# Kernel tuning notes

Measured on AMD Instinct MI355X. Metric: run time of the kernel, lower is better.

Reference implementation:

```python
import jax, jax.numpy as jnp
import numpy as np

N_DIST, H, W, K = 256, 256, 192, 129
DR, DR0, DELTA = 0.2, 0.2, 1e-11


def _dual_exp(d, b1, b2, b3, b4):
    return b1 * np.exp(-b2 * d) + b3 * np.exp(-b4 * d)


def setup_inputs() -> dict:
    key = jax.random.key(0)
    d = (np.arange(N_DIST) + 1.0) * DR                      # distances (cm)
    gaus_amp = _dual_exp(d, 1.0, 0.01, 0.1, 0.001)
    gaus_sig = 0.05 * d + 1.0
    bkg_amp = _dual_exp(d, 0.05, 0.05, 0.01, 0.005)
    bkg_sig = 0.08 * d + 2.0
    xk = np.arange(-(K // 2), K // 2 + 1) * DR / DR0        # (K,) kernel coords
    # gaussian kernel (get_gaus_layer)
    kernel_g = np.sqrt(gaus_amp)[:, None] * np.exp(-xk[None, :] ** 2 / (2 * gaus_sig[:, None] ** 2 + DELTA))
    # background kernels (get_bkg_layers) with emulated splines
    w_f = lambda t: np.exp(-np.abs(t))
    iso_f = lambda t: 1.0 / (1.0 + t ** 2)
    xw = xk[None, :] / bkg_sig[:, None]
    kernel_w = bkg_amp[:, None] * (DR / DR0) * w_f(xw)
    kernel_iso = bkg_amp[:, None] * (DR / DR0) * iso_f(xw)
    # normalization factor (configure)
    xs = np.linspace(-5.0, 5.0, 2001)
    Iw = np.trapz(w_f(xs), xs)
    Iiso = np.trapz(iso_f(xs), xs)
    Nw = 3 * bkg_amp * Iw * bkg_sig
    Niso = bkg_amp * Iiso * bkg_sig
    Ng2 = gaus_amp * 2 * np.pi * gaus_sig ** 2 * (DR0 / DR) ** 2
    norm = (Nw + Niso ** 2 + 1.0) * Ng2
    x = jax.random.uniform(key, (1, N_DIST, H, W), dtype=jnp.float32)
    return {
        "x": x,
        "kernel_g": jnp.asarray(kernel_g, jnp.float32),
        "kernel_w": jnp.asarray(kernel_w, jnp.float32),
        "kernel_iso": jnp.asarray(kernel_iso, jnp.float32),
        "norm": jnp.asarray(norm, jnp.float32),
    }


def _dwconv(x, kern, axis):
    """Depthwise 'same' Conv1d along `axis` of (N,H,W); channels = dim 0."""
    n = x.shape[0]
    perm = (2, 0, 1) if axis == 1 else (1, 0, 2)   # -> (batch, channels=N, length)
    inv = (1, 2, 0) if axis == 1 else (1, 0, 2)
    xb = jnp.transpose(x, perm)
    y = jax.lax.conv_general_dilated(
        xb, kern[:, None, :], (1,), 'SAME',
        feature_group_count=n, dimension_numbers=('NCH', 'OIH', 'NCH'))
    return jnp.transpose(y, inv)


def _rotate(x, ang):
    """Bilinear rotation of (N,S,S) in dims (1,2), zero padding (grid_sample-like)."""
    s = x.shape[1]
    c = (s - 1) * 0.5
    ca, sa = jnp.cos(ang), jnp.sin(ang)
    idx = jnp.arange(s, dtype=x.dtype) - c
    yy, xx = jnp.meshgrid(idx, idx, indexing='ij')
    sy = ca * yy + sa * xx + c   # inverse-rotated source coords
    sx = -sa * yy + ca * xx + c
    y0 = jnp.floor(sy)
    x0 = jnp.floor(sx)
    fy, fx = sy - y0, sx - x0
    y0i, x0i = y0.astype(jnp.int32), x0.astype(jnp.int32)

    def gat(yi, xi):
        valid = (yi >= 0) & (yi < s) & (xi >= 0) & (xi < s)
        v = x[:, jnp.clip(yi, 0, s - 1), jnp.clip(xi, 0, s - 1)]
        return jnp.where(valid, v, 0.0)

    return (gat(y0i, x0i) * (1 - fy) * (1 - fx)
            + gat(y0i, x0i + 1) * (1 - fy) * fx
            + gat(y0i + 1, x0i) * fy * (1 - fx)
            + gat(y0i + 1, x0i + 1) * fy * fx)


def reference(x, kernel_g, kernel_w, kernel_iso, norm):
    out = x[0]                                   # (N, H, W)
    out = _dwconv(out, kernel_g, 1)
    out = _dwconv(out, kernel_g, 2)
    iso = _dwconv(out, kernel_iso, 1)
    iso = _dwconv(iso, kernel_iso, 2)
    n, h, w = out.shape
    pad = (n - w) // 2
    padded = jnp.pad(out, ((0, 0), (0, 0), (pad, pad)))  # (N, H, H) square plane
    tails = jnp.zeros_like(padded)
    for i in range(3):                            # 0, 60, 120 degrees
        ang = float(np.deg2rad(60 * i))
        t = _rotate(padded, ang)
        t = _dwconv(t, kernel_w, 2)
        tails = tails + _rotate(t, -ang)
    tails = tails[:, :, pad:pad + w]
    out = (out + tails + iso) / norm[:, None, None]
    return out[None]
```

## Files before the change

kernel.cpp:

```cpp
#include <hip/hip_runtime.h>
#include <cmath>

#define CN   256
#define HN   256
#define WN   192
#define KN   129
#define RN   64
#define SN   256
#define PADN 32

template <int WD, bool ACC>
__global__ __launch_bounds__(256, 5) void conv_w_lds(const float* __restrict__ in,
                                                     const float* __restrict__ kern,
                                                     float* __restrict__ out) {
    constexpr int PITCH = 97;
    __shared__ float lds[64 * PITCH + 132];
    float* __restrict__ ldsK = lds + 64 * PITCH;
    const int tid = threadIdx.x;
    const int x0  = blockIdx.x * 64;
    const int h0  = blockIdx.y * 64;
    const int c   = blockIdx.z;
    const float* __restrict__ in_c = in + ((size_t)c * HN + h0) * WD;

    if (tid < 132) ldsK[tid] = (tid < KN) ? kern[c * KN + tid] : 0.f;

    const int wv = tid >> 6;
    const int l  = tid & 63;
    const int base  = l * PITCH + wv * 16;
    const int col32 = tid & 31;
    const int r8    = tid >> 5;

    float acc[16];
#pragma unroll
    for (int t = 0; t < 16; ++t) acc[t] = 0.f;

#pragma unroll 1
    for (int s = 0; s < 4; ++s) {
        __syncthreads();
        const int off = x0 + 32 * s - 64;
        if (off >= 0 && off + 96 <= WD) {
#pragma unroll
            for (int m = 0; m < 3; ++m)
#pragma unroll
                for (int k = 0; k < 8; ++k)
                    lds[(r8 + 8 * k) * PITCH + col32 + 32 * m] =
                        in_c[(size_t)(r8 + 8 * k) * WD + off + col32 + 32 * m];
        } else {
#pragma unroll
            for (int m = 0; m < 3; ++m)
#pragma unroll
                for (int k = 0; k < 8; ++k) {
                    int g  = off + col32 + 32 * m;
                    int gc = min(max(g, 0), WD - 1);
                    float v = in_c[(size_t)(r8 + 8 * k) * WD + gc];
                    lds[(r8 + 8 * k) * PITCH + col32 + 32 * m] = (g == gc) ? v : 0.f;
                }
        }
        __syncthreads();

        float H0[16], H1[16], H2[16];
#pragma unroll
        for (int i = 0; i < 16; ++i) H0[i] = lds[base + i];
#pragma unroll
        for (int i = 0; i < 16; ++i) H1[i] = lds[base + 16 + i];

        const float4* __restrict__ k4 = (const float4*)ldsK;
        float4 kc = k4[8 * s];
#pragma unroll
        for (int q = 0; q < 8; ++q) {
            float4 kn = (q < 7) ? k4[8 * s + q + 1] : kc;
#pragma unroll
            for (int u = 0; u < 4; ++u) {
                const int up = 4 * q + u;
                const float kj = (u == 0) ? kc.x : (u == 1) ? kc.y
                               : (u == 2) ? kc.z : kc.w;
#pragma unroll
                for (int t = 0; t < 16; ++t) {
                    const int e = up + t;
                    const float val = (e < 16) ? H0[e]
                                    : (e < 32) ? H1[e - 16] : H2[e - 32];
                    acc[t] = fmaf(val, kj, acc[t]);
                }
            }
            if (q == 0) {
#pragma unroll
                for (int i = 0; i < 16; ++i) H2[i] = lds[base + 32 + i];
            }
            kc = kn;
        }
        if (s == 3) {
            const float k128 = ldsK[128];
#pragma unroll
            for (int t = 0; t < 16; ++t) acc[t] = fmaf(H2[t], k128, acc[t]);
        }
    }

    float4* __restrict__ o4 =
        (float4*)(out + ((size_t)c * HN + h0 + l) * WD + x0 + wv * 16);
#pragma unroll
    for (int q = 0; q < 4; ++q) {
        float4 v;
        v.x = acc[4*q]; v.y = acc[4*q+1]; v.z = acc[4*q+2]; v.w = acc[4*q+3];
        if (ACC) {
            float4 o = o4[q];
            v.x += o.x; v.y += o.y; v.z += o.z; v.w += o.w;
        }
        o4[q] = v;
    }
}

__global__ __launch_bounds__(256, 5) void conv_h_lds(const float* __restrict__ in,
                                                     const float* __restrict__ kern,
                                                     float* __restrict__ out) {
    __shared__ float lds[96 * 64 + 132];
    float* __restrict__ ldsK = lds + 96 * 64;
    const int tid = threadIdx.x;
    const int x0  = blockIdx.x * 64;
    const int h0  = blockIdx.y * 64;
    const int c   = blockIdx.z;
    const float* __restrict__ in_c = in + (size_t)c * HN * WN + x0;

    if (tid < 132) ldsK[tid] = (tid < KN) ? kern[c * KN + tid] : 0.f;

    const int wv = tid >> 6;
    const int l  = tid & 63;
    const int baseRow = wv * 16;
    const int col = tid & 63;
    const int r4  = tid >> 6;

    float acc[16];
#pragma unroll
    for (int t = 0; t < 16; ++t) acc[t] = 0.f;

#pragma unroll 1
    for (int s = 0; s < 4; ++s) {
        __syncthreads();
        const int off = h0 + 32 * s - 64;
        if (off >= 0 && off + 96 <= HN) {
#pragma unroll
            for (int k = 0; k < 24; ++k)
                lds[(r4 + 4 * k) * 64 + col] =
                    in_c[(size_t)(off + r4 + 4 * k) * WN + col];
        } else {
#pragma unroll
            for (int k = 0; k < 24; ++k) {
                int g  = off + r4 + 4 * k;
                int gc = min(max(g, 0), HN - 1);
                float v = in_c[(size_t)gc * WN + col];
                lds[(r4 + 4 * k) * 64 + col] = (g == gc) ? v : 0.f;
            }
        }
        __syncthreads();

        float H0[16], H1[16], H2[16];
#pragma unroll
        for (int i = 0; i < 16; ++i) H0[i] = lds[(baseRow + i) * 64 + l];
#pragma unroll
        for (int i = 0; i < 16; ++i) H1[i] = lds[(baseRow + 16 + i) * 64 + l];

        const float4* __restrict__ k4 = (const float4*)ldsK;
        float4 kc = k4[8 * s];
#pragma unroll
        for (int q = 0; q < 8; ++q) {
            float4 kn = (q < 7) ? k4[8 * s + q + 1] : kc;
#pragma unroll
            for (int u = 0; u < 4; ++u) {
                const int up = 4 * q + u;
                const float kj = (u == 0) ? kc.x : (u == 1) ? kc.y
                               : (u == 2) ? kc.z : kc.w;
#pragma unroll
                for (int t = 0; t < 16; ++t) {
                    const int e = up + t;
                    const float val = (e < 16) ? H0[e]
                                    : (e < 32) ? H1[e - 16] : H2[e - 32];
                    acc[t] = fmaf(val, kj, acc[t]);
                }
            }
            if (q == 0) {
#pragma unroll
                for (int i = 0; i < 16; ++i)
                    H2[i] = lds[(baseRow + 32 + i) * 64 + l];
            }
            kc = kn;
        }
        if (s == 3) {
            const float k128 = ldsK[128];
#pragma unroll
            for (int t = 0; t < 16; ++t) acc[t] = fmaf(H2[t], k128, acc[t]);
        }
    }

    float* __restrict__ ob = out + ((size_t)c * HN + h0 + wv * 16) * WN + x0 + l;
#pragma unroll
    for (int t = 0; t < 16; ++t) ob[(size_t)t * WN] = acc[t];
}

__global__ __launch_bounds__(256) void rot_fwd_k(const float* __restrict__ Cin,
                                                 float* __restrict__ out,
                                                 float ca, float sa) {
    const int jb = blockIdx.x * 128 + threadIdx.x;
    const int i  = blockIdx.y * 8 + threadIdx.y;
    const int c  = blockIdx.z;
    const float cc = (SN - 1) * 0.5f;
    const float yy = (float)i - cc;
    const float* __restrict__ base = Cin + (size_t)c * HN * WN;
    float* __restrict__ orow = out + ((size_t)c * SN + i) * SN;
#pragma unroll
    for (int q = 0; q < 4; ++q) {
        const int j = jb + q * 32;
        float xx = (float)j - cc;
        float sy = ca * yy + sa * xx + cc;
        float sx = -sa * yy + ca * xx + cc;
        float y0f = floorf(sy), x0f = floorf(sx);
        float fy = sy - y0f, fx = sx - x0f;
        int y0 = (int)y0f, x0i = (int)x0f;
        int p  = x0i - PADN;
        int y0c = min(max(y0, 0), HN - 1);
        int y1c = min(max(y0 + 1, 0), HN - 1);
        int p0c = min(max(p, 0), WN - 1);
        int p1c = min(max(p + 1, 0), WN - 1);
        float wy0 = ((unsigned)y0       < (unsigned)HN) ? (1.f - fy) : 0.f;
        float wy1 = ((unsigned)(y0 + 1) < (unsigned)HN) ? fy : 0.f;
        float wx0 = ((unsigned)p        < (unsigned)WN) ? (1.f - fx) : 0.f;
        float wx1 = ((unsigned)(p + 1)  < (unsigned)WN) ? fx : 0.f;
        const float* r0 = base + (size_t)y0c * WN;
        const float* r1 = base + (size_t)y1c * WN;
        float v00 = r0[p0c], v01 = r0[p1c];
        float v10 = r1[p0c], v11 = r1[p1c];
        orow[j] = wy0 * (wx0 * v00 + wx1 * v01) + wy1 * (wx0 * v10 + wx1 * v11);
    }
}

__global__ __launch_bounds__(256) void rot_bwd_k(const float* __restrict__ U,
                                                 float* __restrict__ acc,
                                                 float ca, float sa) {
    const int xb = blockIdx.x * 64 + threadIdx.x;
    const int i  = blockIdx.y * 8 + threadIdx.y;
    const int c  = blockIdx.z;
    const float cc = (SN - 1) * 0.5f;
    const float yy = (float)i - cc;
    const float* __restrict__ base = U + (size_t)c * SN * SN;
    float* __restrict__ arow = acc + ((size_t)c * HN + i) * WN;
#pragma unroll
    for (int q = 0; q < 2; ++q) {
        const int xc = xb + q * 32;
        const int j  = xc + PADN;
        float xx = (float)j - cc;
        float sy = ca * yy + sa * xx + cc;
        float sx = -sa * yy + ca * xx + cc;
        float y0f = floorf(sy), x0f = floorf(sx);
        float fy = sy - y0f, fx = sx - x0f;
        int y0 = (int)y0f, x0i = (int)x0f;
        int y0c = min(max(y0, 0), SN - 1);
        int y1c = min(max(y0 + 1, 0), SN - 1);
        int p0c = min(max(x0i, 0), SN - 1);
        int p1c = min(max(x0i + 1, 0), SN - 1);
        float wy0 = ((unsigned)y0        < (unsigned)SN) ? (1.f - fy) : 0.f;
        float wy1 = ((unsigned)(y0 + 1)  < (unsigned)SN) ? fy : 0.f;
        float wx0 = ((unsigned)x0i       < (unsigned)SN) ? (1.f - fx) : 0.f;
        float wx1 = ((unsigned)(x0i + 1) < (unsigned)SN) ? fx : 0.f;
        const float* r0 = base + (size_t)y0c * SN;
        const float* r1 = base + (size_t)y1c * SN;
        float v00 = r0[p0c], v01 = r0[p1c];
        float v10 = r1[p0c], v11 = r1[p1c];
        arow[xc] += wy0 * (wx0 * v00 + wx1 * v01) + wy1 * (wx0 * v10 + wx1 * v11);
    }
}

__global__ __launch_bounds__(256) void final_k(float* __restrict__ outC,
                                               const float* __restrict__ acc,
                                               const float* __restrict__ norm) {
    size_t i4 = (size_t)blockIdx.x * 256 + threadIdx.x;
    int c = (int)(i4 / (HN * WN / 4));
    float4* o4 = (float4*)outC;
    const float4* a4 = (const float4*)acc;
    float inv = 1.f / norm[c];
    float4 o = o4[i4], a = a4[i4];
    o.x = (o.x + a.x) * inv; o.y = (o.y + a.y) * inv;
    o.z = (o.z + a.z) * inv; o.w = (o.w + a.w) * inv;
    o4[i4] = o;
}

extern "C" void kernel_launch(void* const* d_in, const int* in_sizes, int n_in,
                              void* d_out, int out_size, void* d_ws, size_t ws_size,
                              hipStream_t stream) {
    const float* x    = (const float*)d_in[0];
    const float* kg   = (const float*)d_in[1];
    const float* kw   = (const float*)d_in[2];
    const float* kiso = (const float*)d_in[3];
    const float* norm = (const float*)d_in[4];

    float* C = (float*)d_out;
    float* ws = (float*)d_ws;
    const size_t IMG = (size_t)CN * HN * WN;
    const size_t PSQ = (size_t)CN * SN * SN;
    float* B   = ws;
    float* acc = ws + IMG;
    float* T   = ws + 2 * IMG;
    float* U   = T + PSQ;

    const dim3 blk256(256);
    const dim3 convHGrid(WN / 64, HN / 64, CN);
    const dim3 convW192Grid(WN / 64, HN / 64, CN);
    const dim3 convW256Grid(SN / 64, HN / 64, CN);
    const dim3 rotFGrid(SN / 128, SN / 8, CN), rotBlk(32, 8);
    const dim3 rotBGrid(WN / 64, SN / 8, CN);

    conv_h_lds<<<convHGrid, blk256, 0, stream>>>(x, kg, B);
    conv_w_lds<WN, false><<<convW192Grid, blk256, 0, stream>>>(B, kg, C);
    conv_h_lds<<<convHGrid, blk256, 0, stream>>>(C, kiso, B);
    conv_w_lds<WN, false><<<convW192Grid, blk256, 0, stream>>>(B, kiso, acc);
    conv_w_lds<WN, true><<<convW192Grid, blk256, 0, stream>>>(C, kw, acc);
    const double a1 = 60.0 * M_PI / 180.0, a2 = 120.0 * M_PI / 180.0;
    const float c1 = (float)cos(a1), s1 = (float)sin(a1);
    const float c2 = (float)cos(a2), s2 = (float)sin(a2);

    rot_fwd_k<<<rotFGrid, rotBlk, 0, stream>>>(C, T, c1, s1);
    conv_w_lds<SN, false><<<convW256Grid, blk256, 0, stream>>>(T, kw, U);
    rot_bwd_k<<<rotBGrid, rotBlk, 0, stream>>>(U, acc, c1, -s1);

    rot_fwd_k<<<rotFGrid, rotBlk, 0, stream>>>(C, T, c2, s2);
    conv_w_lds<SN, false><<<convW256Grid, blk256, 0, stream>>>(T, kw, U);
    rot_bwd_k<<<rotBGrid, rotBlk, 0, stream>>>(U, acc, c2, -s2);

    final_k<<<(unsigned)(IMG / 4 / 256), blk256, 0, stream>>>(C, acc, norm);
    (void)in_sizes; (void)n_in; (void)out_size; (void)ws_size;
}
```

Measured before the change: 823.6 us.

## Stage rotation source tiles in LDS and fuse final normalization into last rotation

Rotation kernels now process 64x64 output tiles per block and first stage the rotated footprint (a 92x96 bounding box) of the source plane into shared memory. The bilinear taps are then read from LDS instead of as scattered global loads. The separate final normalization pass is folded into the second backward rotation, which saves one full read/write pass over the image. In exchange, each block loads some padding and boundary elements it never uses, and LDS use per block goes up.

```diff
diff --git a/kernel.cpp b/kernel.cpp
--- a/kernel.cpp
+++ b/kernel.cpp
@@ -8,6 +8,9 @@
 #define RN   64
 #define SN   256
 #define PADN 32
+
+#define BBR 92
+#define BBP 96
 
 template <int WD, bool ACC>
 __global__ __launch_bounds__(256, 5) void conv_w_lds(const float* __restrict__ in,
@@ -195,90 +198,118 @@
     for (int t = 0; t < 16; ++t) ob[(size_t)t * WN] = acc[t];
 }
 
-__global__ __launch_bounds__(256) void rot_fwd_k(const float* __restrict__ Cin,
-                                                 float* __restrict__ out,
-                                                 float ca, float sa) {
-    const int jb = blockIdx.x * 128 + threadIdx.x;
-    const int i  = blockIdx.y * 8 + threadIdx.y;
+__global__ __launch_bounds__(256) void rot_fwd_lds(const float* __restrict__ Cin,
+                                                   float* __restrict__ out,
+                                                   float ca, float sa) {
+    __shared__ float tile[BBR * BBP];
+    const int j0 = blockIdx.x * 64;
+    const int i0 = blockIdx.y * 64;
     const int c  = blockIdx.z;
     const float cc = (SN - 1) * 0.5f;
-    const float yy = (float)i - cc;
+    const float yA = (float)i0 - cc, yB = (float)(i0 + 63) - cc;
+    const float xA = (float)j0 - cc, xB = (float)(j0 + 63) - cc;
+    const float syAA = ca * yA + sa * xA + cc, syAB = ca * yA + sa * xB + cc;
+    const float syBA = ca * yB + sa * xA + cc, syBB = ca * yB + sa * xB + cc;
+    const float sxAA = -sa * yA + ca * xA + cc, sxAB = -sa * yA + ca * xB + cc;
+    const float sxBA = -sa * yB + ca * xA + cc, sxBB = -sa * yB + ca * xB + cc;
+    const int ybase = (int)floorf(fminf(fminf(syAA, syAB), fminf(syBA, syBB))) - 1;
+    const int xbase = (int)floorf(fminf(fminf(sxAA, sxAB), fminf(sxBA, sxBB))) - 1;
+
     const float* __restrict__ base = Cin + (size_t)c * HN * WN;
-    float* __restrict__ orow = out + ((size_t)c * SN + i) * SN;
-#pragma unroll
-    for (int q = 0; q < 4; ++q) {
-        const int j = jb + q * 32;
-        float xx = (float)j - cc;
-        float sy = ca * yy + sa * xx + cc;
-        float sx = -sa * yy + ca * xx + cc;
-        float y0f = floorf(sy), x0f = floorf(sx);
-        float fy = sy - y0f, fx = sx - x0f;
-        int y0 = (int)y0f, x0i = (int)x0f;
-        int p  = x0i - PADN;
-        int y0c = min(max(y0, 0), HN - 1);
-        int y1c = min(max(y0 + 1, 0), HN - 1);
-        int p0c = min(max(p, 0), WN - 1);
-        int p1c = min(max(p + 1, 0), WN - 1);
-        float wy0 = ((unsigned)y0       < (unsigned)HN) ? (1.f - fy) : 0.f;
-        float wy1 = ((unsigned)(y0 + 1) < (unsigned)HN) ? fy : 0.f;
-        float wx0 = ((unsigned)p        < (unsigned)WN) ? (1.f - fx) : 0.f;
-        float wx1 = ((unsigned)(p + 1)  < (unsigned)WN) ? fx : 0.f;
-        const float* r0 = base + (size_t)y0c * WN;
-        const float* r1 = base + (size_t)y1c * WN;
-        float v00 = r0[p0c], v01 = r0[p1c];
-        float v10 = r1[p0c], v11 = r1[p1c];
-        orow[j] = wy0 * (wx0 * v00 + wx1 * v01) + wy1 * (wx0 * v10 + wx1 * v11);
-    }
-}
-
-__global__ __launch_bounds__(256) void rot_bwd_k(const float* __restrict__ U,
-                                                 float* __restrict__ acc,
-                                                 float ca, float sa) {
-    const int xb = blockIdx.x * 64 + threadIdx.x;
-    const int i  = blockIdx.y * 8 + threadIdx.y;
+    for (int t = threadIdx.x; t < BBR * BBP; t += 256) {
+        const int r  = t / BBP;
+        const int q  = t - r * BBP;
+        const int gy = ybase + r;
+        const int gx = xbase + q - PADN;
+        float v = 0.f;
+        if ((unsigned)gy < (unsigned)HN && (unsigned)gx < (unsigned)WN)
+            v = base[(size_t)gy * WN + gx];
+        tile[t] = v;
+    }
+    __syncthreads();
+
+    const int l  = threadIdx.x & 63;
+    const int r0 = threadIdx.x >> 6;
+    const int j  = j0 + l;
+    const float xx = (float)j - cc;
+    float* __restrict__ ocol = out + (size_t)c * SN * SN + j;
+#pragma unroll
+    for (int t = 0; t < 16; ++t) {
+        const int i = i0 + r0 + 4 * t;
+        const float yy = (float)i - cc;
+        const float sy = ca * yy + sa * xx + cc;
+        const float sx = -sa * yy + ca * xx + cc;
+        const float y0f = floorf(sy), x0f = floorf(sx);
+        const float fy = sy - y0f, fx = sx - x0f;
+        const int ly = (int)y0f - ybase;
+        const int lx = (int)x0f - xbase;
+        const float* p = tile + ly * BBP + lx;
+        const float v00 = p[0], v01 = p[1], v10 = p[BBP], v11 = p[BBP + 1];
+        ocol[(size_t)i * SN] = (1.f - fy) * ((1.f - fx) * v00 + fx * v01)
+                             + fy * ((1.f - fx) * v10 + fx * v11);
+    }
+}
+
+template <bool FINAL>
+__global__ __launch_bounds__(256) void rot_bwd_lds(const float* __restrict__ U,
+                                                   float* __restrict__ dst,
+                                                   const float* __restrict__ accIn,
+                                                   const float* __restrict__ norm,
+                                                   float ca, float sa) {
+    __shared__ float tile[BBR * BBP];
+    const int x0 = blockIdx.x * 64;
+    const int i0 = blockIdx.y * 64;
     const int c  = blockIdx.z;
     const float cc = (SN - 1) * 0.5f;
-    const float yy = (float)i - cc;
+    const float yA = (float)i0 - cc, yB = (float)(i0 + 63) - cc;
+    const float xA = (float)(x0 + PADN) - cc, xB = (float)(x0 + PADN + 63) - cc;
+    const float syAA = ca * yA + sa * xA + cc, syAB = ca * yA + sa * xB + cc;
+    const float syBA = ca * yB + sa * xA + cc, syBB = ca * yB + sa * xB + cc;
+    const float sxAA = -sa * yA + ca * xA + cc, sxAB = -sa * yA + ca * xB + cc;
+    const float sxBA = -sa * yB + ca * xA + cc, sxBB = -sa * yB + ca * xB + cc;
+    const int ybase = (int)floorf(fminf(fminf(syAA, syAB), fminf(syBA, syBB))) - 1;
+    const int xbase = (int)floorf(fminf(fminf(sxAA, sxAB), fminf(sxBA, sxBB))) - 1;
+
     const float* __restrict__ base = U + (size_t)c * SN * SN;
-    float* __restrict__ arow = acc + ((size_t)c * HN + i) * WN;
-#pragma unroll
-    for (int q = 0; q < 2; ++q) {
-        const int xc = xb + q * 32;
-        const int j  = xc + PADN;
-        float xx = (float)j - cc;
-        float sy = ca * yy + sa * xx + cc;
-        float sx = -sa * yy + ca * xx + cc;
-        float y0f = floorf(sy), x0f = floorf(sx);
-        float fy = sy - y0f, fx = sx - x0f;
-        int y0 = (int)y0f, x0i = (int)x0f;
-        int y0c = min(max(y0, 0), SN - 1);
-        int y1c = min(max(y0 + 1, 0), SN - 1);
-        int p0c = min(max(x0i, 0), SN - 1);
-        int p1c = min(max(x0i + 1, 0), SN - 1);
-        float wy0 = ((unsigned)y0        < (unsigned)SN) ? (1.f - fy) : 0.f;
-        float wy1 = ((unsigned)(y0 + 1)  < (unsigned)SN) ? fy : 0.f;
-        float wx0 = ((unsigned)x0i       < (unsigned)SN) ? (1.f - fx) : 0.f;
-        float wx1 = ((unsigned)(x0i + 1) < (unsigned)SN) ? fx : 0.f;
-        const float* r0 = base + (size_t)y0c * SN;
-        const float* r1 = base + (size_t)y1c * SN;
-        float v00 = r0[p0c], v01 = r0[p1c];
-        float v10 = r1[p0c], v11 = r1[p1c];
-        arow[xc] += wy0 * (wx0 * v00 + wx1 * v01) + wy1 * (wx0 * v10 + wx1 * v11);
-    }
-}
-
-__global__ __launch_bounds__(256) void final_k(float* __restrict__ outC,
-                                               const float* __restrict__ acc,
-                                               const float* __restrict__ norm) {
-    size_t i4 = (size_t)blockIdx.x * 256 + threadIdx.x;
-    int c = (int)(i4 / (HN * WN / 4));
-    float4* o4 = (float4*)outC;
-    const float4* a4 = (const float4*)acc;
-    float inv = 1.f / norm[c];
-    float4 o = o4[i4], a = a4[i4];
-    o.x = (o.x + a.x) * inv; o.y = (o.y + a.y) * inv;
-    o.z = (o.z + a.z) * inv; o.w = (o.w + a.w) * inv;
-    o4[i4] = o;
+    for (int t = threadIdx.x; t < BBR * BBP; t += 256) {
+        const int r  = t / BBP;
+        const int q  = t - r * BBP;
+        const int gy = ybase + r;
+        const int gx = xbase + q;
+        float v = 0.f;
+        if ((unsigned)gy < (unsigned)SN && (unsigned)gx < (unsigned)SN)
+            v = base[(size_t)gy * SN + gx];
+        tile[t] = v;
+    }
+    __syncthreads();
+
+    const int l  = threadIdx.x & 63;
+    const int r0 = threadIdx.x >> 6;
+    const int xc = x0 + l;
+    const float xx = (float)(xc + PADN) - cc;
+    float inv = 0.f;
+    if constexpr (FINAL) inv = 1.f / norm[c];
+#pragma unroll
+    for (int t = 0; t < 16; ++t) {
+        const int i = i0 + r0 + 4 * t;
+        const float yy = (float)i - cc;
+        const float sy = ca * yy + sa * xx + cc;
+        const float sx = -sa * yy + ca * xx + cc;
+        const float y0f = floorf(sy), x0f = floorf(sx);
+        const float fy = sy - y0f, fx = sx - x0f;
+        const int ly = (int)y0f - ybase;
+        const int lx = (int)x0f - xbase;
+        const float* p = tile + ly * BBP + lx;
+        const float v00 = p[0], v01 = p[1], v10 = p[BBP], v11 = p[BBP + 1];
+        const float val = (1.f - fy) * ((1.f - fx) * v00 + fx * v01)
+                        + fy * ((1.f - fx) * v10 + fx * v11);
+        const size_t idx = ((size_t)c * HN + i) * WN + xc;
+        if constexpr (FINAL) {
+            dst[idx] = (dst[idx] + accIn[idx] + val) * inv;
+        } else {
+            dst[idx] += val;
+        }
+    }
 }
 
 extern "C" void kernel_launch(void* const* d_in, const int* in_sizes, int n_in,
@@ -303,8 +334,8 @@
     const dim3 convHGrid(WN / 64, HN / 64, CN);
     const dim3 convW192Grid(WN / 64, HN / 64, CN);
     const dim3 convW256Grid(SN / 64, HN / 64, CN);
-    const dim3 rotFGrid(SN / 128, SN / 8, CN), rotBlk(32, 8);
-    const dim3 rotBGrid(WN / 64, SN / 8, CN);
+    const dim3 rotFGrid(SN / 64, SN / 64, CN);
+    const dim3 rotBGrid(WN / 64, HN / 64, CN);
 
     conv_h_lds<<<convHGrid, blk256, 0, stream>>>(x, kg, B);
     conv_w_lds<WN, false><<<convW192Grid, blk256, 0, stream>>>(B, kg, C);
@@ -315,14 +346,13 @@
     const float c1 = (float)cos(a1), s1 = (float)sin(a1);
     const float c2 = (float)cos(a2), s2 = (float)sin(a2);
 
-    rot_fwd_k<<<rotFGrid, rotBlk, 0, stream>>>(C, T, c1, s1);
+    rot_fwd_lds<<<rotFGrid, blk256, 0, stream>>>(C, T, c1, s1);
     conv_w_lds<SN, false><<<convW256Grid, blk256, 0, stream>>>(T, kw, U);
-    rot_bwd_k<<<rotBGrid, rotBlk, 0, stream>>>(U, acc, c1, -s1);
-
-    rot_fwd_k<<<rotFGrid, rotBlk, 0, stream>>>(C, T, c2, s2);
+    rot_bwd_lds<false><<<rotBGrid, blk256, 0, stream>>>(U, acc, nullptr, nullptr, c1, -s1);
+
+    rot_fwd_lds<<<rotFGrid, blk256, 0, stream>>>(C, T, c2, s2);
     conv_w_lds<SN, false><<<convW256Grid, blk256, 0, stream>>>(T, kw, U);
-    rot_bwd_k<<<rotBGrid, rotBlk, 0, stream>>>(U, acc, c2, -s2);
-
-    final_k<<<(unsigned)(IMG / 4 / 256), blk256, 0, stream>>>(C, acc, norm);
+    rot_bwd_lds<true><<<rotBGrid, blk256, 0, stream>>>(U, C, acc, norm, c2, -s2);
+
     (void)in_sizes; (void)n_in; (void)out_size; (void)ws_size;
 }
```

Result: faster. 768.4 us (-6.7%).
